# Kernel tuning notes

Hardware: AMD Instinct MI355X
Metric: run time of the kernel (lower is better)

Reference implementation:

```python
import jax, jax.numpy as jnp
import numpy as np

D_MODEL, D_FF, D_NEURON, D_HIDDEN = 512, 2048, 128, 256
PHI_IN = D_NEURON + 1  # 129
EPS = 1e-5


def _ln(x, g, b):
    mu = x.mean(-1, keepdims=True)
    var = ((x - mu) ** 2).mean(-1, keepdims=True)
    return (x - mu) * jax.lax.rsqrt(var + EPS) * g + b


def _gelu(x):
    return jax.nn.gelu(x, approximate=False)


def setup_inputs() -> dict:
    key = jax.random.key(0)
    ks = jax.random.split(key, 16)
    s = 0.02
    inp = {
        'x': jax.random.normal(ks[0], (4, 1024, D_MODEL), jnp.float32),
        'W_in': jax.random.normal(ks[1], (D_FF, D_MODEL), jnp.float32) * s,
        'neuron_vecs': jax.random.normal(ks[2], (D_FF, D_NEURON), jnp.float32) * s,
        'Wr1': jax.random.normal(ks[3], (D_MODEL, D_MODEL), jnp.float32) * s,
        'Wr2': jax.random.normal(ks[4], (D_FF, D_MODEL), jnp.float32) * s,
        'rn_g': jnp.ones((D_MODEL,), jnp.float32),
        'rn_b': jnp.zeros((D_MODEL,), jnp.float32),
        'pW1': jax.random.normal(ks[5], (PHI_IN, D_HIDDEN), jnp.float32) * (1.0 / np.sqrt(PHI_IN)),
        'pb1': jnp.zeros((D_HIDDEN,), jnp.float32),
        'pln1_g': jnp.ones((D_HIDDEN,), jnp.float32),
        'pln1_b': jnp.zeros((D_HIDDEN,), jnp.float32),
        'pW2': jax.random.normal(ks[6], (D_HIDDEN, D_HIDDEN), jnp.float32) * (1.0 / np.sqrt(D_HIDDEN)),
        'pb2': jnp.zeros((D_HIDDEN,), jnp.float32),
        'pln2_g': jnp.ones((D_HIDDEN,), jnp.float32),
        'pln2_b': jnp.zeros((D_HIDDEN,), jnp.float32),
        'rln_g': jnp.ones((D_HIDDEN,), jnp.float32),
        'rln_b': jnp.zeros((D_HIDDEN,), jnp.float32),
        'rW1': jax.random.normal(ks[7], (D_HIDDEN, 2 * D_HIDDEN), jnp.float32) * (1.0 / np.sqrt(D_HIDDEN)),
        'rb1': jnp.zeros((2 * D_HIDDEN,), jnp.float32),
        'rW2': jax.random.normal(ks[8], (2 * D_HIDDEN, D_MODEL), jnp.float32) * (1.0 / np.sqrt(2 * D_HIDDEN)),
        'rb2': jnp.zeros((D_MODEL,), jnp.float32),
        'top_k': 64,
    }
    return inp


def reference(x, W_in, neuron_vecs, Wr1, Wr2, rn_g, rn_b,
              pW1, pb1, pln1_g, pln1_b, pW2, pb2, pln2_g, pln2_b,
              rln_g, rln_b, rW1, rb1, rW2, rb2, top_k):
    batch, seq, d_model = x.shape
    xf = x.reshape(-1, d_model)  # [T, D]

    # Router (MLP variant): LN -> GELU(x @ Wr1^T) -> @ Wr2^T
    h = _gelu(_ln(xf, rn_g, rn_b) @ Wr1.T)
    scores = h @ Wr2.T  # [T, d_ff]
    _, idx = jax.lax.top_k(scores, top_k)  # [T, K]

    # Gather selected neuron params (irregular access)
    W_sel = W_in[idx]           # [T, K, D]
    nv_sel = neuron_vecs[idx]   # [T, K, d_neuron]

    # Per-token activations for selected neurons
    act = _gelu(jnp.einsum('td,tkd->tk', xf, W_sel))  # [T, K]

    # phi: Linear -> LN -> GELU -> Linear -> LN
    phi_in = jnp.concatenate([nv_sel, act[..., None]], axis=-1)  # [T, K, 129]
    hphi = _ln(phi_in @ pW1 + pb1, pln1_g, pln1_b)
    hphi = _gelu(hphi)
    hphi = _ln(hphi @ pW2 + pb2, pln2_g, pln2_b)  # [T, K, d_hidden]

    agg = hphi.sum(axis=1)  # [T, d_hidden]

    # rho: LN -> Linear -> GELU -> (Dropout eval=identity) -> Linear
    r = _ln(agg, rln_g, rln_b)
    r = _gelu(r @ rW1 + rb1)
    out = r @ rW2 + rb2  # [T, d_model]
    return out.reshape(batch, seq, d_model)
```

## Files before the change

kernel.cpp:

```cpp
#include <hip/hip_runtime.h>
#include <cstdint>
#include <cstddef>

typedef unsigned short u16;
typedef float f32x4 __attribute__((ext_vector_type(4)));
typedef short short8 __attribute__((ext_vector_type(8)));
typedef int i32x4 __attribute__((ext_vector_type(4)));


__device__ __forceinline__ float geluf(float v) {
  return 0.5f * v * (1.0f + erff(v * 0.70710678118654752440f));
}

__device__ __forceinline__ float erf_fast(float x) {
  const float ax = fabsf(x);
  const float t = __builtin_amdgcn_rcpf(fmaf(0.3275911f, ax, 1.0f));
  float p = fmaf(1.061405429f, t, -1.453152027f);
  p = fmaf(p, t, 1.421413741f);
  p = fmaf(p, t, -0.284496736f);
  p = fmaf(p, t, 0.254829592f);
  p = p * t;
  const float e = __expf(-ax * ax);
  const float r = fmaf(-p, e, 1.0f);
  return copysignf(r, x);
}
__device__ __forceinline__ float gelu_fast(float v) {
  return 0.5f * v * (1.0f + erf_fast(v * 0.70710678118654752440f));
}

__device__ __forceinline__ u16 f2bf(float f) {
  unsigned u = __float_as_uint(f);
  u = (u + 0x7FFFu + ((u >> 16) & 1u)) >> 16;
  return (u16)u;
}
__device__ __forceinline__ float bf2f(u16 h) {
  return __uint_as_float(((unsigned)h) << 16);
}

__device__ __forceinline__ void waveRed2(float& s, float& s2) {
#pragma unroll
  for (int m = 1; m < 64; m <<= 1) {
    s += __shfl_xor(s, m);
    s2 += __shfl_xor(s2, m);
  }
}

__global__ __launch_bounds__(256) void k_ln512(const float* __restrict__ x,
                                               const float* __restrict__ g,
                                               const float* __restrict__ b,
                                               float* __restrict__ out) {
  __shared__ float red[8];
  const int t = blockIdx.x, tid = threadIdx.x;
  const float v0 = x[(size_t)t * 512 + tid];
  const float v1 = x[(size_t)t * 512 + 256 + tid];
  float s = v0 + v1, s2 = v0 * v0 + v1 * v1;
  waveRed2(s, s2);
  if ((tid & 63) == 0) { red[(tid >> 6) * 2] = s; red[(tid >> 6) * 2 + 1] = s2; }
  __syncthreads();
  s = red[0] + red[2] + red[4] + red[6];
  s2 = red[1] + red[3] + red[5] + red[7];
  const float mu = s * (1.f / 512.f);
  const float var = fmaxf(s2 * (1.f / 512.f) - mu * mu, 0.f);
  const float rstd = 1.f / sqrtf(var + 1e-5f);
  out[(size_t)t * 512 + tid] = (v0 - mu) * rstd * g[tid] + b[tid];
  out[(size_t)t * 512 + 256 + tid] = (v1 - mu) * rstd * g[tid + 256] + b[tid + 256];
}

__global__ __launch_bounds__(256) void k_prep(
    const float* __restrict__ nv, const float* __restrict__ pW1,
    const float* __restrict__ pb1, float* __restrict__ nvphi,
    const float* __restrict__ pW2, u16* __restrict__ pW2T,
    const float* __restrict__ rW1, u16* __restrict__ rW1T,
    const float* __restrict__ rW2, u16* __restrict__ rW2T,
    const float* __restrict__ Wr2, u16* __restrict__ Wr2b) {
  __shared__ float nvs[128];
  const int b = blockIdx.x, tid = threadIdx.x;
  if (b < 2048) {
    const int n = b;
    if (tid < 128) nvs[tid] = nv[n * 128 + tid];
    __syncthreads();
    float s = pb1[tid];
#pragma unroll 4
    for (int i = 0; i < 128; ++i) s = fmaf(nvs[i], pW1[i * 256 + tid], s);
    nvphi[n * 256 + tid] = s;
  } else if (b < 2304) {
    const int n = b - 2048;
    pW2T[n * 256 + tid] = f2bf(pW2[tid * 256 + n]);
  } else if (b < 2816) {
    const int n = b - 2304;
    if (tid < 256) rW1T[(size_t)n * 256 + tid] = f2bf(rW1[(size_t)tid * 512 + n]);
  } else if (b < 3328) {
    const int n = b - 2816;
    for (int k = tid; k < 512; k += 256)
      rW2T[(size_t)n * 512 + k] = f2bf(rW2[(size_t)k * 512 + n]);
  } else {
    const int i = (b - 3328) * 256 + tid;
    Wr2b[i] = f2bf(Wr2[i]);
  }
}

template <int GMODE, bool BF16OUT>
__global__ __launch_bounds__(256) void gemm8f(const float* __restrict__ A,
                                              const float* __restrict__ B,
                                              float* __restrict__ C,
                                              u16* __restrict__ Cb, int M,
                                              int N, int K) {
  __shared__ float As[16][132];
  __shared__ float Bs[16][132];
  const int tid = threadIdx.x;
  const int tm = tid >> 4, tn = tid & 15;
  const int m0 = blockIdx.y * 128, n0 = blockIdx.x * 128;
  const int sr = tid >> 1, sk = (tid & 1) * 8;
  const float* gA = &A[(size_t)(m0 + sr) * K + sk];
  const float* gB = &B[(size_t)(n0 + sr) * K + sk];
  float acc[8][8] = {};
  for (int k0 = 0; k0 < K; k0 += 16) {
    const float4 a0 = *(const float4*)&gA[k0];
    const float4 a1 = *(const float4*)&gA[k0 + 4];
    const float4 b0 = *(const float4*)&gB[k0];
    const float4 b1 = *(const float4*)&gB[k0 + 4];
    __syncthreads();
    As[sk + 0][sr] = a0.x; As[sk + 1][sr] = a0.y; As[sk + 2][sr] = a0.z; As[sk + 3][sr] = a0.w;
    As[sk + 4][sr] = a1.x; As[sk + 5][sr] = a1.y; As[sk + 6][sr] = a1.z; As[sk + 7][sr] = a1.w;
    Bs[sk + 0][sr] = b0.x; Bs[sk + 1][sr] = b0.y; Bs[sk + 2][sr] = b0.z; Bs[sk + 3][sr] = b0.w;
    Bs[sk + 4][sr] = b1.x; Bs[sk + 5][sr] = b1.y; Bs[sk + 6][sr] = b1.z; Bs[sk + 7][sr] = b1.w;
    __syncthreads();
#pragma unroll
    for (int k = 0; k < 16; ++k) {
      float a[8], b[8];
      *(float4*)&a[0] = *(const float4*)&As[k][tm * 8];
      *(float4*)&a[4] = *(const float4*)&As[k][tm * 8 + 4];
      *(float4*)&b[0] = *(const float4*)&Bs[k][tn * 8];
      *(float4*)&b[4] = *(const float4*)&Bs[k][tn * 8 + 4];
#pragma unroll
      for (int i = 0; i < 8; ++i)
#pragma unroll
        for (int j = 0; j < 8; ++j) acc[i][j] = fmaf(a[i], b[j], acc[i][j]);
    }
  }
#pragma unroll
  for (int i = 0; i < 8; ++i) {
    float4 o0, o1;
    float* p0 = (float*)&o0;
    float* p1 = (float*)&o1;
#pragma unroll
    for (int j = 0; j < 4; ++j) {
      float xv = acc[i][j], yv = acc[i][j + 4];
      if (GMODE == 1) { xv = gelu_fast(xv); yv = gelu_fast(yv); }
      if (GMODE == 2) { xv = geluf(xv); yv = geluf(yv); }
      p0[j] = xv; p1[j] = yv;
    }
    const size_t off = (size_t)(m0 + tm * 8 + i) * N + n0 + tn * 8;
    *(float4*)&C[off] = o0;
    *(float4*)&C[off + 4] = o1;
    if (BF16OUT) {
      ushort4 u0, u1;
      u0.x = f2bf(p0[0]); u0.y = f2bf(p0[1]); u0.z = f2bf(p0[2]); u0.w = f2bf(p0[3]);
      u1.x = f2bf(p1[0]); u1.y = f2bf(p1[1]); u1.z = f2bf(p1[2]); u1.w = f2bf(p1[3]);
      *(ushort4*)&Cb[off] = u0;
      *(ushort4*)&Cb[off + 4] = u1;
    }
  }
}

template <int GMODE, bool BIAS, int OUT>
__global__ __launch_bounds__(256) void gemm_mf(const u16* __restrict__ Ahi,
                                               const u16* __restrict__ Bhi,
                                               const float* __restrict__ bias,
                                               void* __restrict__ Cp, int M,
                                               int N, int K) {
  constexpr int ASZ = 64 * 40;
  constexpr int BSZ = 128 * 40;
  __shared__ __align__(16) u16 smem[ASZ + BSZ];
  u16* sAh = smem;
  u16* sBh = smem + ASZ;

  const int tid = threadIdx.x;
  const int w = tid >> 6, lane = tid & 63;
  const int q = lane >> 4, c = lane & 15;
  const int m0 = blockIdx.y * 64, n0 = blockIdx.x * 128;
  const int ra = tid >> 2, ka = (tid & 3) * 8;
  const int rb = tid >> 1, kb = (tid & 1) * 16;
  const u16* gAh = Ahi + (size_t)(m0 + ra) * K + ka;
  const u16* gBh = Bhi + (size_t)(n0 + rb) * K + kb;

  f32x4 acc[8];
#pragma unroll
  for (int ct = 0; ct < 8; ++ct) {
    const float bv = BIAS ? bias[n0 + ct * 16 + c] : 0.f;
    acc[ct] = (f32x4){bv, bv, bv, bv};
  }

  for (int k0 = 0; k0 < K; k0 += 32) {
    const i32x4 vah = *(const i32x4*)(gAh + k0);
    const i32x4 vbh0 = *(const i32x4*)(gBh + k0);
    const i32x4 vbh1 = *(const i32x4*)(gBh + k0 + 8);
    __syncthreads();
    *(i32x4*)&sAh[ra * 40 + ka] = vah;
    *(i32x4*)&sBh[rb * 40 + kb] = vbh0;
    *(i32x4*)&sBh[rb * 40 + kb + 8] = vbh1;
    __syncthreads();
    const int abase = (w * 16 + c) * 40 + q * 8;
    const short8 ah = *(const short8*)&sAh[abase];
#pragma unroll
    for (int ct = 0; ct < 8; ++ct) {
      const int bbase = (ct * 16 + c) * 40 + q * 8;
      const short8 bh = *(const short8*)&sBh[bbase];
      acc[ct] = __builtin_amdgcn_mfma_f32_16x16x32_bf16(ah, bh, acc[ct], 0, 0, 0);
    }
  }
#pragma unroll
  for (int ct = 0; ct < 8; ++ct) {
#pragma unroll
    for (int reg = 0; reg < 4; ++reg) {
      float v = acc[ct][reg];
      if (GMODE == 1) v = gelu_fast(v);
      const size_t off = (size_t)(m0 + w * 16 + q * 4 + reg) * N + n0 + ct * 16 + c;
      if (OUT == 0) ((float*)Cp)[off] = v;
      else          ((u16*)Cp)[off] = f2bf(v);
    }
  }
}

__global__ __launch_bounds__(256) void k_topk_act(
    const u16* __restrict__ scoresb, const float* __restrict__ h,
    const float* __restrict__ Wr2, const float* __restrict__ x,
    const float* __restrict__ W_in, int* __restrict__ idxout,
    float* __restrict__ act) {
  __shared__ float hs[512];
  __shared__ int redc[4];
  __shared__ int cand[160];
  __shared__ float cex[160];
  __shared__ int selidx[64];
  __shared__ unsigned ccnt, cg_cnt, ec;
  __shared__ int eqbuf[64];
  const int t = blockIdx.x, tid = threadIdx.x;
  hs[tid] = h[(size_t)t * 512 + tid];
  hs[tid + 256] = h[(size_t)t * 512 + 256 + tid];
  unsigned key[8];
#pragma unroll
  for (int j = 0; j < 8; ++j) {
    const unsigned u = (unsigned)scoresb[(size_t)t * 2048 + tid + 256 * j];
    key[j] = (u & 0x8000u) ? (0xFFFFu & ~u) : (u | 0x8000u);
  }
  if (tid == 0) ccnt = 0u;
  unsigned lo = 0u, hi = 0xFFFFu;
  while (lo < hi) {
    const unsigned mid = (lo + hi + 1u) >> 1;
    int c = 0;
#pragma unroll
    for (int j = 0; j < 8; ++j) c += (key[j] >= mid);
#pragma unroll
    for (int m = 1; m < 64; m <<= 1) c += __shfl_xor(c, m);
    if ((tid & 63) == 0) redc[tid >> 6] = c;
    __syncthreads();
    const int total = redc[0] + redc[1] + redc[2] + redc[3];
    __syncthreads();
    if (total >= 96) lo = mid; else hi = mid - 1;
  }
#pragma unroll
  for (int j = 0; j < 8; ++j) {
    if (key[j] >= lo) {
      const unsigned pos = atomicAdd(&ccnt, 1u);
      if (pos < 160u) cand[pos] = tid + 256 * j;
    }
  }
  __syncthreads();
  const int cnt = (int)(ccnt < 160u ? ccnt : 160u);
  const int wv = tid >> 6, l = tid & 63;
  for (int ci = wv; ci < cnt; ci += 4) {
    const float* Wr = Wr2 + (size_t)cand[ci] * 512;
    float s = 0.f;
#pragma unroll
    for (int j = 0; j < 8; ++j) s = fmaf(Wr[l + 64 * j], hs[l + 64 * j], s);
#pragma unroll
    for (int m = 1; m < 64; m <<= 1) s += __shfl_xor(s, m);
    if (l == 0) cex[ci] = s;
  }
  __syncthreads();
  unsigned k2 = 0u;
  int myidx = -1;
  const bool valid = tid < cnt;
  if (valid) {
    const unsigned u = __float_as_uint(cex[tid]);
    k2 = (u & 0x80000000u) ? ~u : (u | 0x80000000u);
    myidx = cand[tid];
  }
  if (tid == 0) { cg_cnt = 0u; ec = 0u; }
  unsigned lo2 = 0u, hi2 = 0xFFFFFFFFu;
  while (lo2 < hi2) {
    const unsigned mid = (unsigned)(((unsigned long long)lo2 + hi2 + 1ull) >> 1);
    int c = (valid && k2 >= mid) ? 1 : 0;
#pragma unroll
    for (int m = 1; m < 64; m <<= 1) c += __shfl_xor(c, m);
    if ((tid & 63) == 0) redc[tid >> 6] = c;
    __syncthreads();
    const int total = redc[0] + redc[1] + redc[2] + redc[3];
    __syncthreads();
    if (total >= 64) lo2 = mid; else hi2 = mid - 1;
  }
  if (valid && k2 > lo2) {
    const unsigned pos = atomicAdd(&cg_cnt, 1u);
    idxout[(size_t)t * 64 + pos] = myidx;
    selidx[pos] = myidx;
  } else if (valid && k2 == lo2) {
    const unsigned e = atomicAdd(&ec, 1u);
    if (e < 64u) eqbuf[e] = myidx;
  }
  __syncthreads();
  if (tid == 0) {
    const int cg = (int)cg_cnt;
    int ne = (int)ec; if (ne > 64) ne = 64;
    const int need = 64 - cg;
    for (int i = 1; i < ne; ++i) {
      const int v = eqbuf[i];
      int j = i - 1;
      while (j >= 0 && eqbuf[j] > v) { eqbuf[j + 1] = eqbuf[j]; --j; }
      eqbuf[j + 1] = v;
    }
    for (int i = 0; i < need; ++i) {
      idxout[(size_t)t * 64 + cg + i] = eqbuf[i];
      selidx[cg + i] = eqbuf[i];
    }
  }
  __syncthreads();
  hs[tid] = x[(size_t)t * 512 + tid];
  hs[tid + 256] = x[(size_t)t * 512 + 256 + tid];
  __syncthreads();
  const float4 xa = *(const float4*)&hs[l * 8];
  const float4 xb = *(const float4*)&hs[l * 8 + 4];
  for (int qq = 0; qq < 16; ++qq) {
    const int k = wv * 16 + qq;
    const int n = selidx[k];
    const float* Wr = W_in + (size_t)n * 512 + l * 8;
    const float4 wa = *(const float4*)Wr;
    const float4 wb = *(const float4*)(Wr + 4);
    float s = wa.x * xa.x;
    s = fmaf(wa.y, xa.y, s); s = fmaf(wa.z, xa.z, s); s = fmaf(wa.w, xa.w, s);
    s = fmaf(wb.x, xb.x, s); s = fmaf(wb.y, xb.y, s);
    s = fmaf(wb.z, xb.z, s); s = fmaf(wb.w, xb.w, s);
#pragma unroll
    for (int m = 1; m < 64; m <<= 1) s += __shfl_xor(s, m);
    if (l == 0) act[(size_t)t * 64 + k] = gelu_fast(s);
  }
}

__global__ __launch_bounds__(256, 1) void k_phi(
    const float* __restrict__ nvphi, const float* __restrict__ pW1,
    const float* __restrict__ pln1_g, const float* __restrict__ pln1_b,
    const u16* __restrict__ pW2T, const float* __restrict__ pb2,
    const float* __restrict__ pln2_g, const float* __restrict__ pln2_b,
    const int* __restrict__ idx, const float* __restrict__ act,
    const float* __restrict__ rln_g, const float* __restrict__ rln_b,
    u16* __restrict__ rh) {
  __shared__ __align__(16) u16 h1s[64 * 264];
  __shared__ __align__(16) u16 Bs[64 * 264];
  __shared__ float aggbuf[4 * 256];
  __shared__ float red[8];
  __shared__ int idxs[64];
  __shared__ float acts[64];
  const int tid = threadIdx.x;
  const int t = blockIdx.x;
  const int w = tid >> 6, lane = tid & 63;
  const int q = lane >> 4, c = lane & 15;
  if (tid < 64) {
    idxs[tid] = idx[(size_t)t * 64 + tid];
    acts[tid] = act[(size_t)t * 64 + tid];
  }
  __syncthreads();
  {
    f32x4 w4[4], g1[4], b1[4];
#pragma unroll
    for (int j = 0; j < 4; ++j) {
      w4[j] = *(const f32x4*)&pW1[128 * 256 + c * 16 + j * 4];
      g1[j] = *(const f32x4*)&pln1_g[c * 16 + j * 4];
      b1[j] = *(const f32x4*)&pln1_b[c * 16 + j * 4];
    }
#pragma unroll 1
    for (int rd = 0; rd < 4; ++rd) {
      const int p = w * 16 + rd * 4 + q;
      const int n = idxs[p];
      const float av = acts[p];
      f32x4 v[4];
      float s = 0.f, s2 = 0.f;
#pragma unroll
      for (int j = 0; j < 4; ++j) {
        const f32x4 nv = *(const f32x4*)&nvphi[(size_t)n * 256 + c * 16 + j * 4];
#pragma unroll
        for (int u = 0; u < 4; ++u) {
          v[j][u] = nv[u] + av * w4[j][u];
          s += v[j][u];
          s2 = fmaf(v[j][u], v[j][u], s2);
        }
      }
#pragma unroll
      for (int m = 1; m < 16; m <<= 1) { s += __shfl_xor(s, m); s2 += __shfl_xor(s2, m); }
      const float mu = s * (1.f / 256.f);
      const float var = fmaxf(s2 * (1.f / 256.f) - mu * mu, 0.f);
      const float rstd = 1.f / sqrtf(var + 1e-5f);
      short8 lo, hi;
#pragma unroll
      for (int j = 0; j < 4; ++j)
#pragma unroll
        for (int u = 0; u < 4; ++u) {
          const float hv = gelu_fast((v[j][u] - mu) * rstd * g1[j][u] + b1[j][u]);
          if (j < 2) lo[j * 4 + u] = (short)f2bf(hv);
          else       hi[(j - 2) * 4 + u] = (short)f2bf(hv);
        }
      *(short8*)&h1s[p * 264 + c * 16] = lo;
      *(short8*)&h1s[p * 264 + c * 16 + 8] = hi;
    }
  }
  __syncthreads();
  short8 afr[8];
#pragma unroll
  for (int ks = 0; ks < 8; ++ks)
    afr[ks] = *(const short8*)&h1s[(w * 16 + c) * 264 + ks * 32 + q * 8];
  f32x4 acc[16];
#pragma unroll
  for (int nt = 0; nt < 16; ++nt) {
    const float bz = pb2[nt * 16 + c];
    acc[nt] = (f32x4){bz, bz, bz, bz};
  }
#pragma unroll
  for (int ch = 0; ch < 4; ++ch) {
    __syncthreads();
#pragma unroll
    for (int i = 0; i < 8; ++i) {
      const int cidx = i * 256 + tid;
      const int n = cidx >> 5, kc = cidx & 31;
      *(i32x4*)&Bs[n * 264 + kc * 8] =
          *(const i32x4*)&pW2T[(size_t)(ch * 64 + n) * 256 + kc * 8];
    }
    __syncthreads();
#pragma unroll
    for (int t4 = 0; t4 < 4; ++t4) {
      const int nt = ch * 4 + t4;
#pragma unroll
      for (int ks = 0; ks < 8; ++ks) {
        const short8 bfr = *(const short8*)&Bs[(t4 * 16 + c) * 264 + ks * 32 + q * 8];
        acc[nt] = __builtin_amdgcn_mfma_f32_16x16x32_bf16(afr[ks], bfr, acc[nt], 0, 0, 0);
      }
    }
  }
  float g2v[16], b2v[16];
#pragma unroll
  for (int nt = 0; nt < 16; ++nt) {
    g2v[nt] = pln2_g[nt * 16 + c];
    b2v[nt] = pln2_b[nt * 16 + c];
  }
  float aggl[16];
#pragma unroll
  for (int nt = 0; nt < 16; ++nt) aggl[nt] = 0.f;
#pragma unroll
  for (int reg = 0; reg < 4; ++reg) {
    float s = 0.f, s2 = 0.f;
#pragma unroll
    for (int nt = 0; nt < 16; ++nt) {
      const float vv = acc[nt][reg];
      s += vv;
      s2 = fmaf(vv, vv, s2);
    }
#pragma unroll
    for (int m = 1; m < 16; m <<= 1) { s += __shfl_xor(s, m); s2 += __shfl_xor(s2, m); }
    const float mu = s * (1.f / 256.f);
    const float var = fmaxf(s2 * (1.f / 256.f) - mu * mu, 0.f);
    const float rstd = 1.f / sqrtf(var + 1e-5f);
#pragma unroll
    for (int nt = 0; nt < 16; ++nt) {
      const float vv = acc[nt][reg];
      aggl[nt] += (vv - mu) * rstd * g2v[nt] + b2v[nt];
    }
  }
#pragma unroll
  for (int nt = 0; nt < 16; ++nt) {
    float vs = aggl[nt];
    vs += __shfl_xor(vs, 16);
    vs += __shfl_xor(vs, 32);
    if (q == 0) aggbuf[w * 256 + nt * 16 + c] = vs;
  }
  __syncthreads();
  const float v = aggbuf[tid] + aggbuf[256 + tid] + aggbuf[512 + tid] + aggbuf[768 + tid];
  float s = v, s2 = v * v;
  waveRed2(s, s2);
  if ((tid & 63) == 0) { red[(tid >> 6) * 2] = s; red[(tid >> 6) * 2 + 1] = s2; }
  __syncthreads();
  s = red[0] + red[2] + red[4] + red[6];
  s2 = red[1] + red[3] + red[5] + red[7];
  const float mu = s * (1.f / 256.f);
  const float var = fmaxf(s2 * (1.f / 256.f) - mu * mu, 0.f);
  const float rstd = 1.f / sqrtf(var + 1e-5f);
  rh[(size_t)t * 256 + tid] = f2bf((v - mu) * rstd * rln_g[tid] + rln_b[tid]);
}

extern "C" void kernel_launch(void* const* d_in, const int* in_sizes, int n_in,
                              void* d_out, int out_size, void* d_ws, size_t ws_size,
                              hipStream_t stream) {
  const float* x = (const float*)d_in[0];
  const float* W_in = (const float*)d_in[1];
  const float* nv = (const float*)d_in[2];
  const float* Wr1 = (const float*)d_in[3];
  const float* Wr2 = (const float*)d_in[4];
  const float* rn_g = (const float*)d_in[5];
  const float* rn_b = (const float*)d_in[6];
  const float* pW1 = (const float*)d_in[7];
  const float* pb1 = (const float*)d_in[8];
  const float* pln1_g = (const float*)d_in[9];
  const float* pln1_b = (const float*)d_in[10];
  const float* pW2 = (const float*)d_in[11];
  const float* pb2 = (const float*)d_in[12];
  const float* pln2_g = (const float*)d_in[13];
  const float* pln2_b = (const float*)d_in[14];
  const float* rln_g = (const float*)d_in[15];
  const float* rln_b = (const float*)d_in[16];
  const float* rW1 = (const float*)d_in[17];
  const float* rb1 = (const float*)d_in[18];
  const float* rW2 = (const float*)d_in[19];
  const float* rb2 = (const float*)d_in[20];
  float* out = (float*)d_out;
  const int T = in_sizes[0] / 512;

  float* ws = (float*)d_ws;
  float* xln = ws;    ws += (size_t)T * 512;
  float* h = ws;      ws += (size_t)T * 512;
  float* nvphi = ws;  ws += (size_t)2048 * 256;
  float* actb = ws;   ws += (size_t)T * 64;
  int* idx = (int*)ws;   ws += (size_t)T * 64;
  u16* scoresb = (u16*)ws; ws += (size_t)T * 2048 / 2;
  u16* hb = (u16*)ws;    ws += (size_t)T * 512 / 2;
  u16* Wr2b = (u16*)ws;  ws += (size_t)2048 * 512 / 2;
  u16* pW2T = (u16*)ws;  ws += (size_t)2048 * 256 / 2;
  u16* rh = (u16*)ws;    ws += (size_t)T * 256 / 2;
  u16* t1b = (u16*)ws;   ws += (size_t)T * 512 / 2;
  u16* rW1T = (u16*)ws;  ws += (size_t)512 * 256 / 2;
  u16* rW2T = (u16*)ws;  ws += (size_t)512 * 512 / 2;

  k_prep<<<7424, 256, 0, stream>>>(nv, pW1, pb1, nvphi, pW2, pW2T, rW1, rW1T,
                                   rW2, rW2T, Wr2, Wr2b);
  k_ln512<<<T, 256, 0, stream>>>(x, rn_g, rn_b, xln);
  gemm8f<2, true><<<dim3(512 / 128, T / 128), 256, 0, stream>>>(
      xln, Wr1, h, hb, T, 512, 512);
  gemm_mf<0, false, 1><<<dim3(2048 / 128, T / 64), 256, 0, stream>>>(
      hb, Wr2b, nullptr, scoresb, T, 2048, 512);
  k_topk_act<<<T, 256, 0, stream>>>(scoresb, h, Wr2, x, W_in, idx, actb);
  k_phi<<<T, 256, 0, stream>>>(nvphi, pW1, pln1_g, pln1_b, pW2T, pb2, pln2_g,
                               pln2_b, idx, actb, rln_g, rln_b, rh);
  gemm_mf<1, true, 1><<<dim3(512 / 128, T / 64), 256, 0, stream>>>(
      rh, rW1T, rb1, t1b, T, 512, 256);
  gemm_mf<0, true, 0><<<dim3(512 / 128, T / 64), 256, 0, stream>>>(
      t1b, rW2T, rb2, out, T, 512, 512);
}
```

Before: 479.7 us.

## Split waves into 16-lane groups for gather dot products and prefetch phi rows

The candidate-rescoring and W_in gather dot products now give each 16-lane subgroup one row, with each lane loading 32 contiguous floats as float4s against a register-cached copy of the input vector. This cuts the full-wave shuffle reductions and lets each wave keep four independent row loads in flight. In the phi kernel, all four rounds of neuron-vector loads are issued up front and the round loop is fully unrolled to overlap gather latency. The cost is higher register pressure from the 32-float caches and the 16 prefetched vectors.

```diff
diff --git a/kernel.cpp b/kernel.cpp
--- a/kernel.cpp
+++ b/kernel.cpp
@@ -268,14 +268,25 @@
   __syncthreads();
   const int cnt = (int)(ccnt < 160u ? ccnt : 160u);
   const int wv = tid >> 6, l = tid & 63;
-  for (int ci = wv; ci < cnt; ci += 4) {
-    const float* Wr = Wr2 + (size_t)cand[ci] * 512;
+  const int sub = l >> 4, li = l & 15;
+  float hr[32];
+#pragma unroll
+  for (int j = 0; j < 8; ++j)
+    *(float4*)&hr[j * 4] = *(const float4*)&hs[li * 32 + j * 4];
+  for (int ci = wv * 4 + sub; ci < cnt; ci += 16) {
+    const float* Wr = Wr2 + (size_t)cand[ci] * 512 + li * 32;
     float s = 0.f;
 #pragma unroll
-    for (int j = 0; j < 8; ++j) s = fmaf(Wr[l + 64 * j], hs[l + 64 * j], s);
-#pragma unroll
-    for (int m = 1; m < 64; m <<= 1) s += __shfl_xor(s, m);
-    if (l == 0) cex[ci] = s;
+    for (int j = 0; j < 8; ++j) {
+      const float4 w4 = *(const float4*)(Wr + j * 4);
+      s = fmaf(w4.x, hr[j * 4 + 0], s);
+      s = fmaf(w4.y, hr[j * 4 + 1], s);
+      s = fmaf(w4.z, hr[j * 4 + 2], s);
+      s = fmaf(w4.w, hr[j * 4 + 3], s);
+    }
+#pragma unroll
+    for (int m = 1; m < 16; m <<= 1) s += __shfl_xor(s, m);
+    if (li == 0) cex[ci] = s;
   }
   __syncthreads();
   unsigned k2 = 0u;
@@ -327,21 +338,27 @@
   hs[tid] = x[(size_t)t * 512 + tid];
   hs[tid + 256] = x[(size_t)t * 512 + 256 + tid];
   __syncthreads();
-  const float4 xa = *(const float4*)&hs[l * 8];
-  const float4 xb = *(const float4*)&hs[l * 8 + 4];
-  for (int qq = 0; qq < 16; ++qq) {
-    const int k = wv * 16 + qq;
+  float xr[32];
+#pragma unroll
+  for (int j = 0; j < 8; ++j)
+    *(float4*)&xr[j * 4] = *(const float4*)&hs[li * 32 + j * 4];
+#pragma unroll 1
+  for (int pass = 0; pass < 4; ++pass) {
+    const int k = pass * 16 + wv * 4 + sub;
     const int n = selidx[k];
-    const float* Wr = W_in + (size_t)n * 512 + l * 8;
-    const float4 wa = *(const float4*)Wr;
-    const float4 wb = *(const float4*)(Wr + 4);
-    float s = wa.x * xa.x;
-    s = fmaf(wa.y, xa.y, s); s = fmaf(wa.z, xa.z, s); s = fmaf(wa.w, xa.w, s);
-    s = fmaf(wb.x, xb.x, s); s = fmaf(wb.y, xb.y, s);
-    s = fmaf(wb.z, xb.z, s); s = fmaf(wb.w, xb.w, s);
-#pragma unroll
-    for (int m = 1; m < 64; m <<= 1) s += __shfl_xor(s, m);
-    if (l == 0) act[(size_t)t * 64 + k] = gelu_fast(s);
+    const float* Wr = W_in + (size_t)n * 512 + li * 32;
+    float s = 0.f;
+#pragma unroll
+    for (int j = 0; j < 8; ++j) {
+      const float4 w4 = *(const float4*)(Wr + j * 4);
+      s = fmaf(w4.x, xr[j * 4 + 0], s);
+      s = fmaf(w4.y, xr[j * 4 + 1], s);
+      s = fmaf(w4.z, xr[j * 4 + 2], s);
+      s = fmaf(w4.w, xr[j * 4 + 3], s);
+    }
+#pragma unroll
+    for (int m = 1; m < 16; m <<= 1) s += __shfl_xor(s, m);
+    if (li == 0) act[(size_t)t * 64 + k] = gelu_fast(s);
   }
 }
 
@@ -369,6 +386,14 @@
   }
   __syncthreads();
   {
+    f32x4 nvv[16];
+#pragma unroll
+    for (int rd = 0; rd < 4; ++rd) {
+      const int n = idxs[w * 16 + rd * 4 + q];
+#pragma unroll
+      for (int j = 0; j < 4; ++j)
+        nvv[rd * 4 + j] = *(const f32x4*)&nvphi[(size_t)n * 256 + c * 16 + j * 4];
+    }
     f32x4 w4[4], g1[4], b1[4];
 #pragma unroll
     for (int j = 0; j < 4; ++j) {
@@ -376,19 +401,17 @@
       g1[j] = *(const f32x4*)&pln1_g[c * 16 + j * 4];
       b1[j] = *(const f32x4*)&pln1_b[c * 16 + j * 4];
     }
-#pragma unroll 1
+#pragma unroll
     for (int rd = 0; rd < 4; ++rd) {
       const int p = w * 16 + rd * 4 + q;
-      const int n = idxs[p];
       const float av = acts[p];
       f32x4 v[4];
       float s = 0.f, s2 = 0.f;
 #pragma unroll
       for (int j = 0; j < 4; ++j) {
-        const f32x4 nv = *(const f32x4*)&nvphi[(size_t)n * 256 + c * 16 + j * 4];
 #pragma unroll
         for (int u = 0; u < 4; ++u) {
-          v[j][u] = nv[u] + av * w4[j][u];
+          v[j][u] = nvv[rd * 4 + j][u] + av * w4[j][u];
           s += v[j][u];
           s2 = fmaf(v[j][u], v[j][u], s2);
         }
```

Measured after the change: 541.4 us. 12.9% more time.
